# Performance work log

Hardware: AMD Instinct MI355X
Metric: run time of the kernel (lower is better)

Reference implementation:

```python
import jax, jax.numpy as jnp
import numpy as np

B, N, C, R = 8, 1024, 256, 16


def setup_inputs() -> dict:
    key = jax.random.key(0)
    kq, kk, kwq, kwk, kbq, kbk, kr = jax.random.split(key, 7)
    init = 0.02
    return {
        "query_states": jax.random.normal(kq, (B, N, C), dtype=jnp.float32),
        "key_states": jax.random.normal(kk, (B, N, C), dtype=jnp.float32),
        "W_q": jax.random.normal(kwq, (C, C), dtype=jnp.float32) * init,
        "b_q": jax.random.normal(kbq, (C,), dtype=jnp.float32) * init,
        "W_k": jax.random.normal(kwk, (C, C), dtype=jnp.float32) * init,
        "b_k": jax.random.normal(kbk, (C,), dtype=jnp.float32) * init,
        "R_map": jax.random.normal(kr, (N, N, R), dtype=jnp.float32),
    }


def reference(query_states, key_states, W_q, b_q, W_k, b_k, R_map):
    input_dtype = query_states.dtype
    c = query_states.shape[-1]
    # Q/K linear projections (torch Linear: x @ W.T + b)
    qh = query_states @ W_q.T + b_q  # (B, N, C)
    kh = key_states @ W_k.T + b_k    # (B, N, C)
    # batched QK^T score in fp32 (original casts to float32 before bmm)
    scores = jnp.einsum(
        "bic,bjc->bij", qh.astype(jnp.float32), kh.astype(jnp.float32)
    ) / jnp.sqrt(jnp.asarray(c, jnp.float32))  # (B, N, N)
    # elementwise relation-mask multiply: broadcast over relation axis
    rel_mask = jnp.transpose(R_map, (2, 0, 1))  # (R, N, N)
    relation = scores[:, None, :, :] * rel_mask[None]  # (B, R, N, N)
    return relation.astype(input_dtype)
```

## Files before the change

### kernel.cpp

```cpp
#include <hip/hip_runtime.h>
#include <hip/hip_bf16.h>


typedef float  floatx4 __attribute__((ext_vector_type(4)));
typedef short  shortx8 __attribute__((ext_vector_type(8)));

__device__ __forceinline__ short f2bf(float f) {
    unsigned int u = __builtin_bit_cast(unsigned int, f);
    u += 0x7fffu + ((u >> 16) & 1u);
    return (short)(u >> 16);
}

__global__ __launch_bounds__(64) void proj_kernel(
    const float* __restrict__ Xq, const float* __restrict__ Wq, const float* __restrict__ bq,
    const float* __restrict__ Xk, const float* __restrict__ Wk, const float* __restrict__ bk,
    short* __restrict__ qh, short* __restrict__ kh)
{
    const float* X; const float* W; const float* bias; short* outp;
    if (blockIdx.z == 0) { X = Xq; W = Wq; bias = bq; outp = qh; }
    else                 { X = Xk; W = Wk; bias = bk; outp = kh; }

    const int lane  = threadIdx.x;
    const int row16 = lane & 15;
    const int quad  = lane >> 4;
    const int m0 = blockIdx.x * 16;
    const int c0 = blockIdx.y * 16;

    const float* xr = X + (size_t)(m0 + row16) * 256 + quad * 8;
    const float* wr = W + (size_t)(c0 + row16) * 256 + quad * 8;

    floatx4 acc = {0.f, 0.f, 0.f, 0.f};
#pragma unroll
    for (int k = 0; k < 256; k += 32) {
        float4 a0 = *(const float4*)(xr + k);
        float4 a1 = *(const float4*)(xr + k + 4);
        float4 b0 = *(const float4*)(wr + k);
        float4 b1 = *(const float4*)(wr + k + 4);
        shortx8 af = { f2bf(a0.x), f2bf(a0.y), f2bf(a0.z), f2bf(a0.w),
                       f2bf(a1.x), f2bf(a1.y), f2bf(a1.z), f2bf(a1.w) };
        shortx8 bf = { f2bf(b0.x), f2bf(b0.y), f2bf(b0.z), f2bf(b0.w),
                       f2bf(b1.x), f2bf(b1.y), f2bf(b1.z), f2bf(b1.w) };
        acc = __builtin_amdgcn_mfma_f32_16x16x32_bf16(af, bf, acc, 0, 0, 0);
    }

    const int c = c0 + row16;
    const float bv = bias[c];
#pragma unroll
    for (int r = 0; r < 4; r++) {
        const int m = m0 + quad * 4 + r;
        outp[(size_t)m * 256 + c] = f2bf(acc[r] + bv);
    }
}

__global__ __launch_bounds__(256) void score_mul_kernel(
    const short* __restrict__ qh, const short* __restrict__ kh,
    const float* __restrict__ Rm, float* __restrict__ out)
{
    const int b  = blockIdx.x;
    const int j0 = blockIdx.y * 64;
    const int i0 = blockIdx.z * 64;

    const int tid   = threadIdx.x;
    const int wave  = tid >> 6;
    const int lane  = tid & 63;
    const int row16 = lane & 15;
    const int quad  = lane >> 4;

    __shared__ float s_lds[64 * 68];

    const short* qbase = qh + ((size_t)(b * 1024 + i0 + wave * 16 + row16)) * 256 + quad * 8;
    const short* kbase = kh + ((size_t)(b * 1024 + j0 + row16)) * 256 + quad * 8;

    floatx4 acc[4];
#pragma unroll
    for (int nt = 0; nt < 4; nt++) acc[nt] = floatx4{0.f, 0.f, 0.f, 0.f};

#pragma unroll
    for (int k = 0; k < 256; k += 32) {
        shortx8 af = *(const shortx8*)(qbase + k);
#pragma unroll
        for (int nt = 0; nt < 4; nt++) {
            shortx8 bf = *(const shortx8*)(kbase + (size_t)nt * 16 * 256 + k);
            acc[nt] = __builtin_amdgcn_mfma_f32_16x16x32_bf16(af, bf, acc[nt], 0, 0, 0);
        }
    }

    const float inv = 0.0625f;
#pragma unroll
    for (int nt = 0; nt < 4; nt++) {
#pragma unroll
        for (int r = 0; r < 4; r++) {
            const int il = wave * 16 + quad * 4 + r;
            const int jl = nt * 16 + row16;
            s_lds[il * 68 + jl] = acc[nt][r] * inv;
        }
    }
    __syncthreads();

    const int j = tid & 63;
    const int w = tid >> 6;
    const size_t NN = (size_t)1024 * 1024;

#pragma unroll 2
    for (int ii = 0; ii < 16; ii++) {
        const int il = w * 16 + ii;
        const int i  = i0 + il;
        const float s = s_lds[il * 68 + j];
        const float* rp = Rm + ((size_t)i * 1024 + (j0 + j)) * 16;
        float4 r0 = *(const float4*)(rp);
        float4 r1 = *(const float4*)(rp + 4);
        float4 r2 = *(const float4*)(rp + 8);
        float4 r3 = *(const float4*)(rp + 12);
        float* op = out + ((size_t)(b * 16) * 1024 + i) * 1024 + (j0 + j);
        op[0 * NN]  = s * r0.x;  op[1 * NN]  = s * r0.y;
        op[2 * NN]  = s * r0.z;  op[3 * NN]  = s * r0.w;
        op[4 * NN]  = s * r1.x;  op[5 * NN]  = s * r1.y;
        op[6 * NN]  = s * r1.z;  op[7 * NN]  = s * r1.w;
        op[8 * NN]  = s * r2.x;  op[9 * NN]  = s * r2.y;
        op[10 * NN] = s * r2.z;  op[11 * NN] = s * r2.w;
        op[12 * NN] = s * r3.x;  op[13 * NN] = s * r3.y;
        op[14 * NN] = s * r3.z;  op[15 * NN] = s * r3.w;
    }
}

extern "C" void kernel_launch(void* const* d_in, const int* in_sizes, int n_in,
                              void* d_out, int out_size, void* d_ws, size_t ws_size,
                              hipStream_t stream) {
    const float* q   = (const float*)d_in[0];
    const float* k   = (const float*)d_in[1];
    const float* Wq  = (const float*)d_in[2];
    const float* bq  = (const float*)d_in[3];
    const float* Wk  = (const float*)d_in[4];
    const float* bk  = (const float*)d_in[5];
    const float* Rm  = (const float*)d_in[6];
    float* out = (float*)d_out;

    short* qh = (short*)d_ws;
    short* kh = (short*)d_ws + (size_t)8192 * 256;

    dim3 pgrid(512, 16, 2);
    proj_kernel<<<pgrid, 64, 0, stream>>>(q, Wq, bq, k, Wk, bk, qh, kh);

    dim3 sgrid(8, 16, 16);
    score_mul_kernel<<<sgrid, 256, 0, stream>>>(qh, kh, Rm, out);
}
```

Measured before the change: 719.5 us.

## Vectorize relation stores, remap block order for R_map reuse, widen projection tiles

The score-multiply epilogue is reorganised so each lane handles four adjacent columns and four relation channels, writing 16-byte nontemporal stores instead of scalar stores. Block indices are remapped so the eight batches sharing one (i,j) tile run next to each other, which should let R_map reads hit in cache across batches. The projection kernel now computes four 16-column tiles per wave and reuses the converted X fragment, cutting the grid by four. The cost is more registers per thread and a more complex index mapping.

```diff
diff --git a/kernel.cpp b/kernel.cpp
--- a/kernel.cpp
+++ b/kernel.cpp
@@ -24,31 +24,41 @@
     const int row16 = lane & 15;
     const int quad  = lane >> 4;
     const int m0 = blockIdx.x * 16;
-    const int c0 = blockIdx.y * 16;
+    const int c0 = blockIdx.y * 64;
 
     const float* xr = X + (size_t)(m0 + row16) * 256 + quad * 8;
     const float* wr = W + (size_t)(c0 + row16) * 256 + quad * 8;
 
-    floatx4 acc = {0.f, 0.f, 0.f, 0.f};
+    floatx4 acc[4];
+#pragma unroll
+    for (int nt = 0; nt < 4; nt++) acc[nt] = floatx4{0.f, 0.f, 0.f, 0.f};
+
 #pragma unroll
     for (int k = 0; k < 256; k += 32) {
         float4 a0 = *(const float4*)(xr + k);
         float4 a1 = *(const float4*)(xr + k + 4);
-        float4 b0 = *(const float4*)(wr + k);
-        float4 b1 = *(const float4*)(wr + k + 4);
         shortx8 af = { f2bf(a0.x), f2bf(a0.y), f2bf(a0.z), f2bf(a0.w),
                        f2bf(a1.x), f2bf(a1.y), f2bf(a1.z), f2bf(a1.w) };
-        shortx8 bf = { f2bf(b0.x), f2bf(b0.y), f2bf(b0.z), f2bf(b0.w),
-                       f2bf(b1.x), f2bf(b1.y), f2bf(b1.z), f2bf(b1.w) };
-        acc = __builtin_amdgcn_mfma_f32_16x16x32_bf16(af, bf, acc, 0, 0, 0);
+#pragma unroll
+        for (int nt = 0; nt < 4; nt++) {
+            const float* w0 = wr + (size_t)nt * 16 * 256 + k;
+            float4 b0 = *(const float4*)(w0);
+            float4 b1 = *(const float4*)(w0 + 4);
+            shortx8 bf = { f2bf(b0.x), f2bf(b0.y), f2bf(b0.z), f2bf(b0.w),
+                           f2bf(b1.x), f2bf(b1.y), f2bf(b1.z), f2bf(b1.w) };
+            acc[nt] = __builtin_amdgcn_mfma_f32_16x16x32_bf16(af, bf, acc[nt], 0, 0, 0);
+        }
     }
 
-    const int c = c0 + row16;
-    const float bv = bias[c];
 #pragma unroll
-    for (int r = 0; r < 4; r++) {
-        const int m = m0 + quad * 4 + r;
-        outp[(size_t)m * 256 + c] = f2bf(acc[r] + bv);
+    for (int nt = 0; nt < 4; nt++) {
+        const int c = c0 + nt * 16 + row16;
+        const float bv = bias[c];
+#pragma unroll
+        for (int r = 0; r < 4; r++) {
+            const int m = m0 + quad * 4 + r;
+            outp[(size_t)m * 256 + c] = f2bf(acc[nt][r] + bv);
+        }
     }
 }
 
@@ -56,9 +66,11 @@
     const short* __restrict__ qh, const short* __restrict__ kh,
     const float* __restrict__ Rm, float* __restrict__ out)
 {
-    const int b  = blockIdx.x;
-    const int j0 = blockIdx.y * 64;
-    const int i0 = blockIdx.z * 64;
+    const int lin  = blockIdx.x + 8 * (blockIdx.y + 16 * blockIdx.z);
+    const int b    = (lin >> 3) & 7;
+    const int tile = (lin & 7) + ((lin >> 6) << 3);
+    const int j0 = (tile & 15) * 64;
+    const int i0 = (tile >> 4) * 64;
 
     const int tid   = threadIdx.x;
     const int wave  = tid >> 6;
@@ -97,29 +109,33 @@
     }
     __syncthreads();
 
-    const int j = tid & 63;
-    const int w = tid >> 6;
+    const int j4 = lane & 15;
+    const int rg = lane >> 4;
+    const int w  = tid >> 6;
     const size_t NN = (size_t)1024 * 1024;
+
+    float* ob = out + ((size_t)(b * 16 + rg * 4)) * NN + j0 + j4 * 4;
 
 #pragma unroll 2
     for (int ii = 0; ii < 16; ii++) {
         const int il = w * 16 + ii;
         const int i  = i0 + il;
-        const float s = s_lds[il * 68 + j];
-        const float* rp = Rm + ((size_t)i * 1024 + (j0 + j)) * 16;
-        float4 r0 = *(const float4*)(rp);
-        float4 r1 = *(const float4*)(rp + 4);
-        float4 r2 = *(const float4*)(rp + 8);
-        float4 r3 = *(const float4*)(rp + 12);
-        float* op = out + ((size_t)(b * 16) * 1024 + i) * 1024 + (j0 + j);
-        op[0 * NN]  = s * r0.x;  op[1 * NN]  = s * r0.y;
-        op[2 * NN]  = s * r0.z;  op[3 * NN]  = s * r0.w;
-        op[4 * NN]  = s * r1.x;  op[5 * NN]  = s * r1.y;
-        op[6 * NN]  = s * r1.z;  op[7 * NN]  = s * r1.w;
-        op[8 * NN]  = s * r2.x;  op[9 * NN]  = s * r2.y;
-        op[10 * NN] = s * r2.z;  op[11 * NN] = s * r2.w;
-        op[12 * NN] = s * r3.x;  op[13 * NN] = s * r3.y;
-        op[14 * NN] = s * r3.z;  op[15 * NN] = s * r3.w;
+        floatx4 s4 = *(const floatx4*)&s_lds[il * 68 + j4 * 4];
+        const float* rp = Rm + ((size_t)i * 1024 + j0 + j4 * 4) * 16 + rg * 4;
+        floatx4 q0 = *(const floatx4*)(rp);
+        floatx4 q1 = *(const floatx4*)(rp + 16);
+        floatx4 q2 = *(const floatx4*)(rp + 32);
+        floatx4 q3 = *(const floatx4*)(rp + 48);
+        float* op = ob + (size_t)i * 1024;
+
+        floatx4 v0 = { s4[0] * q0[0], s4[1] * q1[0], s4[2] * q2[0], s4[3] * q3[0] };
+        __builtin_nontemporal_store(v0, (floatx4*)(op));
+        floatx4 v1 = { s4[0] * q0[1], s4[1] * q1[1], s4[2] * q2[1], s4[3] * q3[1] };
+        __builtin_nontemporal_store(v1, (floatx4*)(op + NN));
+        floatx4 v2 = { s4[0] * q0[2], s4[1] * q1[2], s4[2] * q2[2], s4[3] * q3[2] };
+        __builtin_nontemporal_store(v2, (floatx4*)(op + 2 * NN));
+        floatx4 v3 = { s4[0] * q0[3], s4[1] * q1[3], s4[2] * q2[3], s4[3] * q3[3] };
+        __builtin_nontemporal_store(v3, (floatx4*)(op + 3 * NN));
     }
 }
 
@@ -138,7 +154,7 @@
     short* qh = (short*)d_ws;
     short* kh = (short*)d_ws + (size_t)8192 * 256;
 
-    dim3 pgrid(512, 16, 2);
+    dim3 pgrid(512, 4, 2);
     proj_kernel<<<pgrid, 64, 0, stream>>>(q, Wq, bq, k, Wk, bk, qh, kh);
 
     dim3 sgrid(8, 16, 16);
```

New measurement: 683.4 us. 1.05x faster.
